# Kernel optimization log

Hardware: AMD Instinct MI355X
Metric: run time of the kernel (lower is better)

The kernel has to match this reference:

```python
import jax, jax.numpy as jnp
import numpy as np

NUM_HEADS = 12
LN_EPS = 1e-5


def _layernorm(t, w, b):
    # LayerNorm over last dim (head_dim), biased variance as in torch
    mu = jnp.mean(t, axis=-1, keepdims=True)
    var = jnp.mean(jnp.square(t - mu), axis=-1, keepdims=True)
    return (t - mu) * jax.lax.rsqrt(var + LN_EPS) * w + b


def _apply_rope(t, cos, sin):
    # t: [B, H, S, D]; cos/sin: [S, D//2]; interleaved complex pairs (torch view_as_complex)
    tr = t[..., 0::2]
    ti = t[..., 1::2]
    c = cos[None, None, :, :]
    s = sin[None, None, :, :]
    out_r = tr * c - ti * s
    out_i = tr * s + ti * c
    return jnp.stack([out_r, out_i], axis=-1).reshape(t.shape)


def setup_inputs() -> dict:
    key = jax.random.key(0)
    ks = jax.random.split(key, 6)
    B, N, C = 16, 1024, 768
    H = NUM_HEADS
    D = C // H  # 64
    P, L = 1, 32
    rot_len = N - P - L  # 991
    x = jax.random.normal(ks[0], (B, N, C), dtype=jnp.float32)
    # rotary frequencies (llama-style)
    inv_freq = 1.0 / (10000.0 ** (np.arange(0, D, 2, dtype=np.float32) / D))
    angles = np.arange(rot_len, dtype=np.float32)[:, None] * inv_freq[None, :]
    cos = jnp.asarray(np.cos(angles))
    sin = jnp.asarray(np.sin(angles))
    # parameters (qkv_bias=False, qk_norm=True)
    w_qkv = jax.random.normal(ks[1], (C, 3 * C), dtype=jnp.float32) * (C ** -0.5)
    q_ln_w = jnp.ones((D,), jnp.float32)
    q_ln_b = jnp.zeros((D,), jnp.float32)
    k_ln_w = jnp.ones((D,), jnp.float32)
    k_ln_b = jnp.zeros((D,), jnp.float32)
    w_proj = jax.random.normal(ks[2], (C, C), dtype=jnp.float32) * (C ** -0.5)
    b_proj = jnp.zeros((C,), jnp.float32)
    return {
        "x": x, "cos": cos, "sin": sin,
        "w_qkv": w_qkv,
        "q_ln_w": q_ln_w, "q_ln_b": q_ln_b,
        "k_ln_w": k_ln_w, "k_ln_b": k_ln_b,
        "w_proj": w_proj, "b_proj": b_proj,
        "num_prefix_tokens": 1, "num_latent_tokens": 32,
    }


def reference(x, cos, sin, w_qkv, q_ln_w, q_ln_b, k_ln_w, k_ln_b, w_proj, b_proj,
              num_prefix_tokens, num_latent_tokens):
    B, N, C = x.shape
    H = NUM_HEADS
    D = C // H
    P, L = num_prefix_tokens, num_latent_tokens
    scale = D ** -0.5

    qkv = (x @ w_qkv).reshape(B, N, 3, H, D)
    qkv = jnp.transpose(qkv, (2, 0, 3, 1, 4))  # [3, B, H, N, D]
    q, k, v = qkv[0], qkv[1], qkv[2]

    q = _layernorm(q, q_ln_w, q_ln_b)
    k = _layernorm(k, k_ln_w, k_ln_b)

    # partial RoPE: only the middle [P : N-L] tokens are rotated
    q_rot = _apply_rope(q[:, :, P:N - L], cos, sin)
    k_rot = _apply_rope(k[:, :, P:N - L], cos, sin)
    q = jnp.concatenate([q[:, :, :P], q_rot, q[:, :, N - L:]], axis=2)
    k = jnp.concatenate([k[:, :, :P], k_rot, k[:, :, N - L:]], axis=2)

    attn = jnp.einsum("bhqd,bhkd->bhqk", q * scale, k)
    attn = jax.nn.softmax(attn, axis=-1)
    out = jnp.einsum("bhqk,bhkd->bhqd", attn, v)
    out = jnp.transpose(out, (0, 2, 1, 3)).reshape(B, N, C)
    return out @ w_proj + b_proj
```

## Files before the change

kernel.cpp:

```cpp
#include <hip/hip_runtime.h>
#include <hip/hip_bf16.h>

typedef __attribute__((ext_vector_type(8))) short v8s;
typedef __attribute__((ext_vector_type(4))) short v4s;
typedef __attribute__((ext_vector_type(4))) float f32x4;

__device__ __forceinline__ float bf2f(short s){
  unsigned u = ((unsigned)(unsigned short)s) << 16;
  float f; __builtin_memcpy(&f, &u, 4); return f;
}
__device__ __forceinline__ short f2bf(float f){
  unsigned u; __builtin_memcpy(&u, &f, 4);
  unsigned r = (u + 0x7FFFu + ((u >> 16) & 1u)) >> 16;
  return (short)r;
}
__device__ __forceinline__ unsigned cvtpk(float a, float b){
  unsigned r;
  asm("v_cvt_pk_bf16_f32 %0, %1, %2" : "=v"(r) : "v"(a), "v"(b));
  return r;
}

__device__ __forceinline__ void gload16(const void* g, void* l){
  __builtin_amdgcn_global_load_lds((const __attribute__((address_space(1))) void*)g,
                                   (__attribute__((address_space(3))) void*)l, 16, 0, 0);
}

__global__ __launch_bounds__(256) void k_cast8(const float* __restrict__ in,
                                               short* __restrict__ out, long n){
  long i = ((long)blockIdx.x * 256 + threadIdx.x) * 8;
  long stride = (long)gridDim.x * 256 * 8;
  for (; i < n; i += stride){
    float4 a = *(const float4*)(in + i);
    float4 b = *(const float4*)(in + i + 4);
    v8s v;
    v[0]=f2bf(a.x); v[1]=f2bf(a.y); v[2]=f2bf(a.z); v[3]=f2bf(a.w);
    v[4]=f2bf(b.x); v[5]=f2bf(b.y); v[6]=f2bf(b.z); v[7]=f2bf(b.w);
    *(v8s*)(out + i) = v;
  }
}

__global__ __launch_bounds__(256) void k_tcast(const float* __restrict__ in,
                                               short* __restrict__ out, int R, int Cc){
  __shared__ float T[32][33];
  int tx = threadIdx.x & 31, ty = threadIdx.x >> 5;
  int r0 = blockIdx.x * 32, c0 = blockIdx.y * 32;
  #pragma unroll
  for (int p = 0; p < 4; p++){
    int r = ty + p*8;
    T[r][tx] = in[(long)(r0 + r)*Cc + c0 + tx];
  }
  __syncthreads();
  #pragma unroll
  for (int p = 0; p < 4; p++){
    int r = ty + p*8;
    out[(long)(c0 + r)*R + r0 + tx] = f2bf(T[tx][r]);
  }
}

template<int OUT_MODE>
__global__ __launch_bounds__(256) void k_gemm(const short* __restrict__ A,
                                              const short* __restrict__ Bt,
                                              void* __restrict__ Cout,
                                              const float* __restrict__ bias,
                                              int M, int N, int K){
  __shared__ short As[128*64];
  __shared__ short Bs[128*64];
  int row0 = blockIdx.x * 128, col0 = blockIdx.y * 128;
  int t = threadIdx.x;
  int lane = t & 63, w = t >> 6;
  int g = lane >> 4, r16 = lane & 15;
  int wr = w >> 1, wc = w & 1;
  int rsw = (r16 & 7) << 3;
  int srow = t >> 3;
  int scol = ((t & 7) * 8) ^ ((srow & 7) << 3);
  f32x4 acc[4][4];
  #pragma unroll
  for (int mi = 0; mi < 4; mi++)
    #pragma unroll
    for (int ni = 0; ni < 4; ni++)
      acc[mi][ni] = (f32x4){0.f,0.f,0.f,0.f};

  for (int kt = 0; kt < K; kt += 64){
    #pragma unroll
    for (int p = 0; p < 4; p++){
      int rr = p*32 + srow;
      gload16(&A[(long)(row0 + rr)*K + kt + scol], &As[(p*256 + w*64)*8]);
    }
    #pragma unroll
    for (int p = 0; p < 4; p++){
      int rr = p*32 + srow;
      gload16(&Bt[(long)(col0 + rr)*K + kt + scol], &Bs[(p*256 + w*64)*8]);
    }
    __syncthreads();
    #pragma unroll
    for (int ks = 0; ks < 2; ks++){
      v8s af[4], bfr[4];
      #pragma unroll
      for (int mi = 0; mi < 4; mi++)
        af[mi] = *(const v8s*)&As[(wr*64 + mi*16 + r16)*64 + ((ks*32 + g*8) ^ rsw)];
      #pragma unroll
      for (int ni = 0; ni < 4; ni++)
        bfr[ni] = *(const v8s*)&Bs[(wc*64 + ni*16 + r16)*64 + ((ks*32 + g*8) ^ rsw)];
      __builtin_amdgcn_s_setprio(1);
      #pragma unroll
      for (int mi = 0; mi < 4; mi++)
        #pragma unroll
        for (int ni = 0; ni < 4; ni++)
          acc[mi][ni] = __builtin_amdgcn_mfma_f32_16x16x32_bf16(af[mi], bfr[ni], acc[mi][ni], 0, 0, 0);
      __builtin_amdgcn_s_setprio(0);
    }
    __syncthreads();
  }
  #pragma unroll
  for (int mi = 0; mi < 4; mi++)
    #pragma unroll
    for (int ni = 0; ni < 4; ni++){
      int rbase = row0 + wr*64 + mi*16 + g*4;
      int cc = col0 + wc*64 + ni*16 + r16;
      #pragma unroll
      for (int j = 0; j < 4; j++){
        float v = acc[mi][ni][j];
        if (OUT_MODE == 0)
          ((short*)Cout)[(long)(rbase + j)*N + cc] = f2bf(v);
        else
          ((float*)Cout)[(long)(rbase + j)*N + cc] = v + bias[cc];
      }
    }
}

__global__ __launch_bounds__(256) void k_lnrope(const short* __restrict__ QKV,
     const float* __restrict__ cosT, const float* __restrict__ sinT,
     const float* __restrict__ qw, const float* __restrict__ qb,
     const float* __restrict__ kw, const float* __restrict__ kb,
     short* __restrict__ Qb, short* __restrict__ Kb, short* __restrict__ Vt){
  __shared__ short Vs[64][72];
  int blk = blockIdx.x;
  int ntile = blk & 15, h = (blk >> 4) % 12, b = blk / 192;
  int t = threadIdx.x;
  int tl = t >> 2, ch = t & 3;
  int n = ntile*64 + tl;
  long row = (long)(b*1024 + n) * 2304;
  int d0 = ch * 16;
  long outrow = ((long)(b*12 + h)*1024 + n) * 64;

  #pragma unroll
  for (int sel = 0; sel < 2; sel++){
    const short* src = &QKV[row + sel*768 + h*64 + d0];
    float f[16];
    v8s a0 = *(const v8s*)src;
    v8s a1 = *(const v8s*)(src + 8);
    #pragma unroll
    for (int i = 0; i < 8; i++){ f[i] = bf2f(a0[i]); f[8+i] = bf2f(a1[i]); }
    float s1 = 0.f, s2 = 0.f;
    #pragma unroll
    for (int i = 0; i < 16; i++){ s1 += f[i]; s2 += f[i]*f[i]; }
    s1 += __shfl_xor(s1, 1); s2 += __shfl_xor(s2, 1);
    s1 += __shfl_xor(s1, 2); s2 += __shfl_xor(s2, 2);
    float mu = s1 * (1.0f/64.0f);
    float var = s2 * (1.0f/64.0f) - mu*mu;
    float rs = rsqrtf(var + 1e-5f);
    const float* wp = sel ? kw : qw;
    const float* bp = sel ? kb : qb;
    #pragma unroll
    for (int i = 0; i < 16; i++) f[i] = (f[i] - mu)*rs*wp[d0+i] + bp[d0+i];
    if (n >= 1 && n < 992){
      int pos = n - 1;
      const float* cp = &cosT[pos*32 + ch*8];
      const float* sp = &sinT[pos*32 + ch*8];
      #pragma unroll
      for (int i = 0; i < 8; i++){
        float c = cp[i], s = sp[i];
        float tr = f[2*i], ti = f[2*i+1];
        f[2*i]   = tr*c - ti*s;
        f[2*i+1] = tr*s + ti*c;
      }
    }
    if (sel == 0){
      #pragma unroll
      for (int i = 0; i < 16; i++) f[i] *= 0.18033688011112042f;
    }
    v8s o0, o1;
    #pragma unroll
    for (int i = 0; i < 8; i++){ o0[i] = f2bf(f[i]); o1[i] = f2bf(f[8+i]); }
    short* dst = sel ? &Kb[outrow + d0] : &Qb[outrow + d0];
    *(v8s*)dst = o0;
    *(v8s*)(dst + 8) = o1;
  }
  {
    const short* vsrc = &QKV[row + 1536 + h*64 + d0];
    *(v8s*)&Vs[tl][d0]     = *(const v8s*)vsrc;
    *(v8s*)&Vs[tl][d0 + 8] = *(const v8s*)(vsrc + 8);
  }
  __syncthreads();
  {
    int d = tl, nch = ch;
    v8s o0, o1;
    #pragma unroll
    for (int i = 0; i < 8; i++){ o0[i] = Vs[nch*16 + i][d]; o1[i] = Vs[nch*16 + 8 + i][d]; }
    long vrow = ((long)(b*12 + h)*64 + d)*1024 + ntile*64 + nch*16;
    *(v8s*)&Vt[vrow]     = o0;
    *(v8s*)&Vt[vrow + 8] = o1;
  }
}

__global__ __launch_bounds__(512) void k_attn(const short* __restrict__ Qb,
                                              const short* __restrict__ Kb,
                                              const short* __restrict__ Vt,
                                              short* __restrict__ O){
  __shared__ short Ks[2][64*64];
  __shared__ short Vts[2][64*64];
  int blk = blockIdx.x;
  int qt = blk & 7, h = (blk >> 3) % 12, b = blk / 96;
  long bh = b*12 + h;
  int t = threadIdx.x, lane = t & 63, w = t >> 6;
  int g = lane >> 4, r16 = lane & 15;
  int rsw = (r16 & 7) << 3;
  int q0 = qt*128 + w*16;

  int srow = t >> 3;
  int scol = ((t & 7) * 8) ^ ((srow & 7) << 3);
  const short* Ksrc = &Kb[(bh*1024 + srow)*64 + scol];
  const short* Vsrc = &Vt[(bh*64 + srow)*1024 + scol];
  int lbase = w*512;

  gload16(Ksrc, &Ks[0][lbase]);
  gload16(Vsrc, &Vts[0][lbase]);

  v8s bq[2];
  #pragma unroll
  for (int tt = 0; tt < 2; tt++)
    bq[tt] = *(const v8s*)&Qb[(bh*1024 + q0 + r16)*64 + tt*32 + g*8];

  f32x4 oacc[4];
  #pragma unroll
  for (int t2 = 0; t2 < 4; t2++) oacc[t2] = (f32x4){0.f,0.f,0.f,0.f};
  float m_run = -1e30f, l_part = 0.f;

  asm volatile("s_waitcnt vmcnt(0)" ::: "memory");
  __builtin_amdgcn_s_barrier();
  asm volatile("" ::: "memory");

  for (int it = 0; it < 16; ++it){
    int cur = it & 1;
    if (it < 15){
      int kt = (it + 1) * 64;
      gload16(Ksrc + (long)kt*64, &Ks[cur^1][lbase]);
      gload16(Vsrc + kt,          &Vts[cur^1][lbase]);
    }
    const short* KsC  = &Ks[cur][0];
    const short* VtsC = &Vts[cur][0];

    f32x4 sacc[4];
    #pragma unroll
    for (int f = 0; f < 4; f++) sacc[f] = (f32x4){0.f,0.f,0.f,0.f};
    #pragma unroll
    for (int tt = 0; tt < 2; tt++){
      v8s ak[4];
      #pragma unroll
      for (int f = 0; f < 4; f++)
        ak[f] = *(const v8s*)&KsC[(f*16 + r16)*64 + ((tt*32 + g*8) ^ rsw)];
      __builtin_amdgcn_s_setprio(1);
      #pragma unroll
      for (int f = 0; f < 4; f++)
        sacc[f] = __builtin_amdgcn_mfma_f32_16x16x32_bf16(ak[f], bq[tt], sacc[f], 0, 0, 0);
      __builtin_amdgcn_s_setprio(0);
    }
    float mf[4];
    #pragma unroll
    for (int f = 0; f < 4; f++)
      mf[f] = fmaxf(fmaxf(sacc[f][0], sacc[f][1]), fmaxf(sacc[f][2], sacc[f][3]));
    float mt_loc = fmaxf(fmaxf(mf[0], mf[1]), fmaxf(mf[2], mf[3]));
    if (!__all(mt_loc - m_run <= 8.0f)){
      float mt = fmaxf(mt_loc, __shfl_xor(mt_loc, 16));
      mt = fmaxf(mt, __shfl_xor(mt, 32));
      float m_new = fmaxf(m_run, mt);
      float alpha = exp2f(m_run - m_new);
      float aj4[4];
      #pragma unroll
      for (int j = 0; j < 4; j++) aj4[j] = __shfl(alpha, 4*g + j, 64);
      #pragma unroll
      for (int t2 = 0; t2 < 4; t2++)
        #pragma unroll
        for (int j = 0; j < 4; j++) oacc[t2][j] *= aj4[j];
      l_part *= alpha;
      m_run = m_new;
    }
    float p[4][4];
    float ls[4];
    #pragma unroll
    for (int f = 0; f < 4; f++){
      #pragma unroll
      for (int j = 0; j < 4; j++) p[f][j] = exp2f(sacc[f][j] - m_run);
      ls[f] = (p[f][0] + p[f][1]) + (p[f][2] + p[f][3]);
    }
    l_part += (ls[0] + ls[1]) + (ls[2] + ls[3]);

    unsigned d00 = cvtpk(p[0][0], p[0][1]), d01 = cvtpk(p[0][2], p[0][3]);
    unsigned d10 = cvtpk(p[1][0], p[1][1]), d11 = cvtpk(p[1][2], p[1][3]);
    unsigned d20 = cvtpk(p[2][0], p[2][1]), d21 = cvtpk(p[2][2], p[2][3]);
    unsigned d30 = cvtpk(p[3][0], p[3][1]), d31 = cvtpk(p[3][2], p[3][3]);
    union PU { v8s s; unsigned u[4]; };
    PU pa0, pa1;
    pa0.u[0]=d00; pa0.u[1]=d01; pa0.u[2]=d10; pa0.u[3]=d11;
    pa1.u[0]=d20; pa1.u[1]=d21; pa1.u[2]=d30; pa1.u[3]=d31;

    #pragma unroll
    for (int t2 = 0; t2 < 4; t2++){
      int vrow = (t2*16 + r16)*64;
      #pragma unroll
      for (int kb = 0; kb < 2; kb++){
        union VU { v8s s; v4s h[2]; } vb;
        vb.h[0] = *(const v4s*)&VtsC[vrow + ((kb*32 + g*4) ^ rsw)];
        vb.h[1] = *(const v4s*)&VtsC[vrow + ((kb*32 + 16 + g*4) ^ rsw)];
        __builtin_amdgcn_s_setprio(1);
        oacc[t2] = __builtin_amdgcn_mfma_f32_16x16x32_bf16(kb ? pa1.s : pa0.s, vb.s, oacc[t2], 0, 0, 0);
        __builtin_amdgcn_s_setprio(0);
      }
    }
    asm volatile("s_waitcnt vmcnt(0)" ::: "memory");
    __builtin_amdgcn_s_barrier();
    asm volatile("" ::: "memory");
  }
  float l_tot = l_part;
  l_tot += __shfl_xor(l_tot, 16);
  l_tot += __shfl_xor(l_tot, 32);
  float linv = 1.0f / l_tot;
  float lj[4];
  #pragma unroll
  for (int j = 0; j < 4; j++) lj[j] = __shfl(linv, 4*g + j, 64);
  #pragma unroll
  for (int t2 = 0; t2 < 4; t2++)
    #pragma unroll
    for (int j = 0; j < 4; j++){
      float v = oacc[t2][j] * lj[j];
      O[((long)b*1024 + q0 + 4*g + j)*768 + h*64 + t2*16 + r16] = f2bf(v);
    }
}

extern "C" void kernel_launch(void* const* d_in, const int* in_sizes, int n_in,
                              void* d_out, int out_size, void* d_ws, size_t ws_size,
                              hipStream_t stream) {
  const float* x      = (const float*)d_in[0];
  const float* cosT   = (const float*)d_in[1];
  const float* sinT   = (const float*)d_in[2];
  const float* w_qkv  = (const float*)d_in[3];
  const float* q_ln_w = (const float*)d_in[4];
  const float* q_ln_b = (const float*)d_in[5];
  const float* k_ln_w = (const float*)d_in[6];
  const float* k_ln_b = (const float*)d_in[7];
  const float* w_proj = (const float*)d_in[8];
  const float* b_proj = (const float*)d_in[9];

  char* ws = (char*)d_ws;
  short* Xb       = (short*)(ws);
  short* Wqkv_bt  = (short*)(ws + 25165824);
  short* Wproj_bt = (short*)(ws + 28704768);
  short* QKV      = (short*)(ws + 29884416);
  short* Qb       = (short*)(ws + 105381888);
  short* Kb       = (short*)(ws + 130547712);
  short* Vt       = (short*)(ws + 155713536);
  short* O        = (short*)(ws + 180879360);

  k_cast8<<<6144, 256, 0, stream>>>(x, Xb, 12582912L);
  k_tcast<<<dim3(24, 72), 256, 0, stream>>>(w_qkv, Wqkv_bt, 768, 2304);
  k_tcast<<<dim3(24, 24), 256, 0, stream>>>(w_proj, Wproj_bt, 768, 768);
  k_gemm<0><<<dim3(128, 18), 256, 0, stream>>>(Xb, Wqkv_bt, QKV, nullptr, 16384, 2304, 768);
  k_lnrope<<<3072, 256, 0, stream>>>(QKV, cosT, sinT, q_ln_w, q_ln_b, k_ln_w, k_ln_b, Qb, Kb, Vt);
  k_attn<<<1536, 512, 0, stream>>>(Qb, Kb, Vt, O);
  k_gemm<1><<<dim3(128, 6), 256, 0, stream>>>(O, Wproj_bt, d_out, b_proj, 16384, 768, 768);
}
```

Baseline: 354.5 us.

## Use 128-key tiles in attention and pre-permute V to enable single 16-byte LDS reads

Doubles the key/value tile per pipeline stage from 64 to 128 keys, halving the number of barriers and waitcnt stalls per block. It processes the tile as two 64-key sub-steps of online softmax. The V-transpose kernel now writes V columns in a permuted order, so the attention kernel reads each PV operand with one 16-byte LDS load instead of two 8-byte loads. The setprio toggles are also hoisted around the whole PV loop. The cost is double the LDS use per block, which may reduce occupancy.

New measurement: 354.8 us. About the same (+0.1%).

```diff
diff --git a/kernel.cpp b/kernel.cpp
--- a/kernel.cpp
+++ b/kernel.cpp
@@ -197,9 +197,13 @@
     v8s o0, o1;
     #pragma unroll
     for (int i = 0; i < 8; i++){ o0[i] = Vs[nch*16 + i][d]; o1[i] = Vs[nch*16 + 8 + i][d]; }
-    long vrow = ((long)(b*12 + h)*64 + d)*1024 + ntile*64 + nch*16;
-    *(v8s*)&Vt[vrow]     = o0;
-    *(v8s*)&Vt[vrow + 8] = o1;
+    long vbase = ((long)(b*12 + h)*64 + d)*1024 + ntile*64 + (nch>>1)*32 + (nch&1)*4;
+    union { v8s s; v4s h2[2]; } u0, u1;
+    u0.s = o0; u1.s = o1;
+    *(v4s*)&Vt[vbase]      = u0.h2[0];
+    *(v4s*)&Vt[vbase + 8]  = u0.h2[1];
+    *(v4s*)&Vt[vbase + 16] = u1.h2[0];
+    *(v4s*)&Vt[vbase + 24] = u1.h2[1];
   }
 }
 
@@ -207,8 +211,8 @@
                                               const short* __restrict__ Kb,
                                               const short* __restrict__ Vt,
                                               short* __restrict__ O){
-  __shared__ short Ks[2][64*64];
-  __shared__ short Vts[2][64*64];
+  __shared__ short Ks[2][128*64];
+  __shared__ short Vts[2][64*128];
   int blk = blockIdx.x;
   int qt = blk & 7, h = (blk >> 3) % 12, b = blk / 96;
   long bh = b*12 + h;
@@ -219,12 +223,17 @@
 
   int srow = t >> 3;
   int scol = ((t & 7) * 8) ^ ((srow & 7) << 3);
-  const short* Ksrc = &Kb[(bh*1024 + srow)*64 + scol];
-  const short* Vsrc = &Vt[(bh*64 + srow)*1024 + scol];
+  const short* KsrcB = &Kb[(bh*1024 + srow)*64 + scol];
+  int sdv = t >> 4;
+  int sslot = t & 15;
+  int scolv = (sslot >> 3)*64 + (((sslot & 7)*8) ^ ((sdv & 7) << 3));
+  const short* VsrcB = &Vt[(bh*64 + sdv)*1024 + scolv];
   int lbase = w*512;
 
-  gload16(Ksrc, &Ks[0][lbase]);
-  gload16(Vsrc, &Vts[0][lbase]);
+  gload16(KsrcB,                 &Ks[0][lbase]);
+  gload16(KsrcB + 4096,          &Ks[0][4096 + lbase]);
+  gload16(VsrcB,                 &Vts[0][lbase]);
+  gload16(VsrcB + 32768,         &Vts[0][4096 + lbase]);
 
   v8s bq[2];
   #pragma unroll
@@ -240,82 +249,86 @@
   __builtin_amdgcn_s_barrier();
   asm volatile("" ::: "memory");
 
-  for (int it = 0; it < 16; ++it){
+  for (int it = 0; it < 8; ++it){
     int cur = it & 1;
-    if (it < 15){
-      int kt = (it + 1) * 64;
-      gload16(Ksrc + (long)kt*64, &Ks[cur^1][lbase]);
-      gload16(Vsrc + kt,          &Vts[cur^1][lbase]);
+    if (it < 7){
+      int kt = (it + 1) * 128;
+      gload16(KsrcB + (long)kt*64,          &Ks[cur^1][lbase]);
+      gload16(KsrcB + (long)kt*64 + 4096,   &Ks[cur^1][4096 + lbase]);
+      gload16(VsrcB + kt,                   &Vts[cur^1][lbase]);
+      gload16(VsrcB + 32768 + kt,           &Vts[cur^1][4096 + lbase]);
     }
     const short* KsC  = &Ks[cur][0];
     const short* VtsC = &Vts[cur][0];
 
-    f32x4 sacc[4];
-    #pragma unroll
-    for (int f = 0; f < 4; f++) sacc[f] = (f32x4){0.f,0.f,0.f,0.f};
-    #pragma unroll
-    for (int tt = 0; tt < 2; tt++){
-      v8s ak[4];
+    #pragma unroll
+    for (int sub = 0; sub < 2; sub++){
+      int ksub = sub*4096;
+      f32x4 sacc[4];
+      #pragma unroll
+      for (int f = 0; f < 4; f++) sacc[f] = (f32x4){0.f,0.f,0.f,0.f};
+      #pragma unroll
+      for (int tt = 0; tt < 2; tt++){
+        v8s ak[4];
+        #pragma unroll
+        for (int f = 0; f < 4; f++)
+          ak[f] = *(const v8s*)&KsC[ksub + (f*16 + r16)*64 + ((tt*32 + g*8) ^ rsw)];
+        __builtin_amdgcn_s_setprio(1);
+        #pragma unroll
+        for (int f = 0; f < 4; f++)
+          sacc[f] = __builtin_amdgcn_mfma_f32_16x16x32_bf16(ak[f], bq[tt], sacc[f], 0, 0, 0);
+        __builtin_amdgcn_s_setprio(0);
+      }
+      float mf[4];
       #pragma unroll
       for (int f = 0; f < 4; f++)
-        ak[f] = *(const v8s*)&KsC[(f*16 + r16)*64 + ((tt*32 + g*8) ^ rsw)];
+        mf[f] = fmaxf(fmaxf(sacc[f][0], sacc[f][1]), fmaxf(sacc[f][2], sacc[f][3]));
+      float mt_loc = fmaxf(fmaxf(mf[0], mf[1]), fmaxf(mf[2], mf[3]));
+      if (!__all(mt_loc - m_run <= 8.0f)){
+        float mt = fmaxf(mt_loc, __shfl_xor(mt_loc, 16));
+        mt = fmaxf(mt, __shfl_xor(mt, 32));
+        float m_new = fmaxf(m_run, mt);
+        float alpha = exp2f(m_run - m_new);
+        float aj4[4];
+        #pragma unroll
+        for (int j = 0; j < 4; j++) aj4[j] = __shfl(alpha, 4*g + j, 64);
+        #pragma unroll
+        for (int t2 = 0; t2 < 4; t2++)
+          #pragma unroll
+          for (int j = 0; j < 4; j++) oacc[t2][j] *= aj4[j];
+        l_part *= alpha;
+        m_run = m_new;
+      }
+      float p[4][4];
+      float ls[4];
+      #pragma unroll
+      for (int f = 0; f < 4; f++){
+        #pragma unroll
+        for (int j = 0; j < 4; j++) p[f][j] = exp2f(sacc[f][j] - m_run);
+        ls[f] = (p[f][0] + p[f][1]) + (p[f][2] + p[f][3]);
+      }
+      l_part += (ls[0] + ls[1]) + (ls[2] + ls[3]);
+
+      unsigned d00 = cvtpk(p[0][0], p[0][1]), d01 = cvtpk(p[0][2], p[0][3]);
+      unsigned d10 = cvtpk(p[1][0], p[1][1]), d11 = cvtpk(p[1][2], p[1][3]);
+      unsigned d20 = cvtpk(p[2][0], p[2][1]), d21 = cvtpk(p[2][2], p[2][3]);
+      unsigned d30 = cvtpk(p[3][0], p[3][1]), d31 = cvtpk(p[3][2], p[3][3]);
+      union PU { v8s s; unsigned u[4]; };
+      PU pa0, pa1;
+      pa0.u[0]=d00; pa0.u[1]=d01; pa0.u[2]=d10; pa0.u[3]=d11;
+      pa1.u[0]=d20; pa1.u[1]=d21; pa1.u[2]=d30; pa1.u[3]=d31;
+
       __builtin_amdgcn_s_setprio(1);
       #pragma unroll
-      for (int f = 0; f < 4; f++)
-        sacc[f] = __builtin_amdgcn_mfma_f32_16x16x32_bf16(ak[f], bq[tt], sacc[f], 0, 0, 0);
+      for (int t2 = 0; t2 < 4; t2++){
+        int vrow = (t2*16 + r16)*128 + sub*64;
+        #pragma unroll
+        for (int kb = 0; kb < 2; kb++){
+          v8s vbv = *(const v8s*)&VtsC[vrow + ((kb*32 + g*8) ^ rsw)];
+          oacc[t2] = __builtin_amdgcn_mfma_f32_16x16x32_bf16(kb ? pa1.s : pa0.s, vbv, oacc[t2], 0, 0, 0);
+        }
+      }
       __builtin_amdgcn_s_setprio(0);
-    }
-    float mf[4];
-    #pragma unroll
-    for (int f = 0; f < 4; f++)
-      mf[f] = fmaxf(fmaxf(sacc[f][0], sacc[f][1]), fmaxf(sacc[f][2], sacc[f][3]));
-    float mt_loc = fmaxf(fmaxf(mf[0], mf[1]), fmaxf(mf[2], mf[3]));
-    if (!__all(mt_loc - m_run <= 8.0f)){
-      float mt = fmaxf(mt_loc, __shfl_xor(mt_loc, 16));
-      mt = fmaxf(mt, __shfl_xor(mt, 32));
-      float m_new = fmaxf(m_run, mt);
-      float alpha = exp2f(m_run - m_new);
-      float aj4[4];
-      #pragma unroll
-      for (int j = 0; j < 4; j++) aj4[j] = __shfl(alpha, 4*g + j, 64);
-      #pragma unroll
-      for (int t2 = 0; t2 < 4; t2++)
-        #pragma unroll
-        for (int j = 0; j < 4; j++) oacc[t2][j] *= aj4[j];
-      l_part *= alpha;
-      m_run = m_new;
-    }
-    float p[4][4];
-    float ls[4];
-    #pragma unroll
-    for (int f = 0; f < 4; f++){
-      #pragma unroll
-      for (int j = 0; j < 4; j++) p[f][j] = exp2f(sacc[f][j] - m_run);
-      ls[f] = (p[f][0] + p[f][1]) + (p[f][2] + p[f][3]);
-    }
-    l_part += (ls[0] + ls[1]) + (ls[2] + ls[3]);
-
-    unsigned d00 = cvtpk(p[0][0], p[0][1]), d01 = cvtpk(p[0][2], p[0][3]);
-    unsigned d10 = cvtpk(p[1][0], p[1][1]), d11 = cvtpk(p[1][2], p[1][3]);
-    unsigned d20 = cvtpk(p[2][0], p[2][1]), d21 = cvtpk(p[2][2], p[2][3]);
-    unsigned d30 = cvtpk(p[3][0], p[3][1]), d31 = cvtpk(p[3][2], p[3][3]);
-    union PU { v8s s; unsigned u[4]; };
-    PU pa0, pa1;
-    pa0.u[0]=d00; pa0.u[1]=d01; pa0.u[2]=d10; pa0.u[3]=d11;
-    pa1.u[0]=d20; pa1.u[1]=d21; pa1.u[2]=d30; pa1.u[3]=d31;
-
-    #pragma unroll
-    for (int t2 = 0; t2 < 4; t2++){
-      int vrow = (t2*16 + r16)*64;
-      #pragma unroll
-      for (int kb = 0; kb < 2; kb++){
-        union VU { v8s s; v4s h[2]; } vb;
-        vb.h[0] = *(const v4s*)&VtsC[vrow + ((kb*32 + g*4) ^ rsw)];
-        vb.h[1] = *(const v4s*)&VtsC[vrow + ((kb*32 + 16 + g*4) ^ rsw)];
-        __builtin_amdgcn_s_setprio(1);
-        oacc[t2] = __builtin_amdgcn_mfma_f32_16x16x32_bf16(kb ? pa1.s : pa0.s, vb.s, oacc[t2], 0, 0, 0);
-        __builtin_amdgcn_s_setprio(0);
-      }
     }
     asm volatile("s_waitcnt vmcnt(0)" ::: "memory");
     __builtin_amdgcn_s_barrier();
```
